# Performance work log

Hardware: AMD Instinct MI355X
Metric: run time of the kernel (lower is better)

Reference implementation:

```python
import jax, jax.numpy as jnp
import numpy as np

EPS = 1e-5
NEG_SLOPE = 0.2  # torch LeakyReLU default in DGCNN-style SharedMLPs


def knn_idx(p, k):
    # p: [B, 3, N]; returns idx [B, N, k] of k nearest neighbors (incl. self)
    inner = jnp.einsum('bdn,bdm->bnm', p, p)           # [B,N,N]
    sq = jnp.sum(p * p, axis=1)                         # [B,N]
    neg_dist = 2.0 * inner - sq[:, :, None] - sq[:, None, :]
    return jax.lax.top_k(neg_dist, k)[1]                # [B,N,k]


def smlp1d(x, w, b, g, bt):
    # x: [B,C,N]; 1x1 conv + BatchNorm1d (batch stats) + LeakyReLU
    y = jnp.einsum('bcn,oc->bon', x, w) + b[None, :, None]
    m = y.mean(axis=(0, 2), keepdims=True)
    v = y.var(axis=(0, 2), keepdims=True)
    y = g[None, :, None] * (y - m) * jax.lax.rsqrt(v + EPS) + bt[None, :, None]
    return jax.nn.leaky_relu(y, NEG_SLOPE)


def edgeconv(x, idx, w, b, g, bt):
    # x: [B,C,N], idx: [B,N,k] -> [B,O,N]
    B = x.shape[0]
    xT = jnp.transpose(x, (0, 2, 1))                    # [B,N,C]
    nb = xT[jnp.arange(B)[:, None, None], idx]          # [B,N,k,C] gather
    ctr = jnp.broadcast_to(xT[:, :, None, :], nb.shape)
    feat = jnp.concatenate([nb - ctr, ctr], axis=-1)    # [B,N,k,2C]
    y = jnp.einsum('bnkc,oc->bnko', feat, w) + b        # 1x1 conv2d
    m = y.mean(axis=(0, 1, 2), keepdims=True)
    v = y.var(axis=(0, 1, 2), keepdims=True)
    y = g * (y - m) * jax.lax.rsqrt(v + EPS) + bt
    y = jax.nn.leaky_relu(y, NEG_SLOPE)
    y = jnp.max(y, axis=2)                              # max over k -> [B,N,O]
    return jnp.transpose(y, (0, 2, 1))                  # [B,O,N]


def setup_inputs() -> dict:
    key = jax.random.key(0)
    ks = jax.random.split(key, 16)
    B, N, K = 2, 8192, 20
    C_in = 1024 + 3 * 64  # emb_dims + n_edgeconvs_backbone*64 = 1216
    OUT = 50

    def lin(k, o, c):
        return jax.random.normal(k, (o, c), jnp.float32) * (1.0 / np.sqrt(c))

    return {
        'x': jax.random.normal(ks[0], (B, C_in, N), jnp.float32),
        'p': jax.random.normal(ks[1], (B, 3, N), jnp.float32),
        # smlp1: 1216 -> 256
        'w1': lin(ks[2], 256, C_in), 'b1': jnp.zeros((256,), jnp.float32),
        'g1': jnp.ones((256,), jnp.float32), 'bt1': jnp.zeros((256,), jnp.float32),
        # edgeconv: 512 -> 256
        'we': lin(ks[3], 256, 512), 'be': jnp.zeros((256,), jnp.float32),
        'ge': jnp.ones((256,), jnp.float32), 'bte': jnp.zeros((256,), jnp.float32),
        # smlp2 part 1: 256 -> 256
        'w2': lin(ks[4], 256, 256), 'b2': jnp.zeros((256,), jnp.float32),
        'g2': jnp.ones((256,), jnp.float32), 'bt2': jnp.zeros((256,), jnp.float32),
        # smlp2 part 2: 256 -> 128
        'w3': lin(ks[5], 128, 256), 'b3': jnp.zeros((128,), jnp.float32),
        'g3': jnp.ones((128,), jnp.float32), 'bt3': jnp.zeros((128,), jnp.float32),
        # final conv1d: 128 -> 50
        'wf': lin(ks[6], OUT, 128), 'bf': jnp.zeros((OUT,), jnp.float32),
    }


def reference(x, p, w1, b1, g1, bt1, we, be, ge, bte,
              w2, b2, g2, bt2, w3, b3, g3, bt3, wf, bf):
    K = 20
    h = smlp1d(x, w1, b1, g1, bt1)              # [B,256,N]
    idx = knn_idx(p, K)                          # [B,N,K]
    h = edgeconv(h, idx, we, be, ge, bte)        # [B,256,N]
    h = smlp1d(h, w2, b2, g2, bt2)               # Dropout2d: identity (eval)
    h = smlp1d(h, w3, b3, g3, bt3)               # [B,128,N]
    return jnp.einsum('bcn,oc->bon', h, wf) + bf[None, :, None]  # [B,50,N]
```

## Files before the change

kernel.cpp:

```cpp
#include <hip/hip_runtime.h>

typedef unsigned short u16;
typedef unsigned int   u32;
typedef unsigned long long u64;
typedef __attribute__((ext_vector_type(4))) float f4;
typedef __attribute__((ext_vector_type(8))) short s8;
typedef __attribute__((ext_vector_type(4))) int   i4v;
typedef __attribute__((ext_vector_type(4))) unsigned short u16x4;

#define DEV __device__ __forceinline__

DEV u16 f2b(float f) {
  u32 u = __float_as_uint(f);
  return (u16)((u + 0x7FFFu + ((u >> 16) & 1u)) >> 16);
}
DEV float b2f(u16 h) { return __uint_as_float(((u32)h) << 16); }

#define OFF_STATS 0L
#define OFF_W1B   65536L
#define OFF_WEAB  688128L
#define OFF_W2B   950272L
#define OFF_W3B   1081344L
#define OFF_IDX   1146880L
#define OFF_XT    4194304L
#define OFF_Y1    44040192L
#define OFF_Y2    4194304L
#define OFF_EMAX  23068672L
#define OFF_EMIN  41943040L
#define OFF_Y3    4194304L
#define OFF_Y4    23068672L
#define WS_NEED   71303168L

__global__ __launch_bounds__(256) void k_convw(
    const float* __restrict__ w1, const float* __restrict__ we,
    const float* __restrict__ w2, const float* __restrict__ w3,
    u16* __restrict__ w1b, u16* __restrict__ weABb,
    u16* __restrict__ w2b, u16* __restrict__ w3b)
{
  int i = blockIdx.x * 256 + threadIdx.x;
  if (i < 311296) { w1b[i] = f2b(w1[i]); return; }
  i -= 311296;
  if (i < 131072) {
    int o = i >> 8, c = i & 255;
    float v = (o < 256) ? we[o * 512 + c]
                        : we[(o - 256) * 512 + 256 + c] - we[(o - 256) * 512 + c];
    weABb[i] = f2b(v); return;
  }
  i -= 131072;
  if (i < 65536) { w2b[i] = f2b(w2[i]); return; }
  i -= 65536;
  if (i < 32768) { w3b[i] = f2b(w3[i]); }
}

__global__ __launch_bounds__(256) void k_xt(const float* __restrict__ x, u16* __restrict__ xt)
{
  __shared__ float t[64][65];
  const int b = blockIdx.z, ct = blockIdx.y, nt = blockIdx.x;
  const int tx = threadIdx.x & 63, ty = threadIdx.x >> 6;
  const float* xb = x + (long)b * 1216 * 8192;
#pragma unroll
  for (int i = 0; i < 16; ++i) {
    int c = ct * 64 + ty + i * 4;
    t[ty + i * 4][tx] = xb[(long)c * 8192 + nt * 64 + tx];
  }
  __syncthreads();
  u16* xtb = xt + (long)b * 8192 * 1216;
#pragma unroll
  for (int i = 0; i < 16; ++i) {
    int n = nt * 64 + ty + i * 4;
    xtb[(long)n * 1216 + ct * 64 + tx] = f2b(t[tx][ty + i * 4]);
  }
}

__global__ __launch_bounds__(512, 1) void k_knn(const float* __restrict__ p, int* __restrict__ idxOut)
{
  __shared__ f4 pq[8192];
  __shared__ u16 cand[8][8][120];
  __shared__ double ckeyv[8][120];
  const int tid = threadIdx.x, lane = tid & 63, w = tid >> 6;
  const int blk = blockIdx.x;
  const int b = blk >> 7;
  const int qbase = ((blk & 127) << 6) + (w << 3);
  const float* px = p + (long)b * 24576;
  const float* py = px + 8192;
  const float* pz = px + 16384;
  for (int t4 = tid; t4 < 2048; t4 += 512) {
    f4 x4 = *(const f4*)(px + t4 * 4);
    f4 y4 = *(const f4*)(py + t4 * 4);
    f4 z4 = *(const f4*)(pz + t4 * 4);
#pragma unroll
    for (int j = 0; j < 4; ++j) {
      float X = x4[j], Yv = y4[j], Z = z4[j];
      float s = fmaf(X, X, fmaf(Yv, Yv, Z * Z));
      f4 v; v[0] = X; v[1] = Yv; v[2] = Z; v[3] = s;
      pq[t4 * 4 + j] = v;
    }
  }
  __syncthreads();
  float qx2[8], qy2[8], qz2[8];
#pragma unroll
  for (int j = 0; j < 8; ++j) {
    f4 Q = pq[qbase + j];
    qx2[j] = Q[0] + Q[0]; qy2[j] = Q[1] + Q[1]; qz2[j] = Q[2] + Q[2];
  }
  float mx[8];
#pragma unroll
  for (int j = 0; j < 8; ++j) mx[j] = -3.0e38f;
#pragma unroll 4
  for (int t = 0; t < 128; ++t) {
    f4 c = pq[(t << 6) + lane];
#pragma unroll
    for (int j = 0; j < 8; ++j) {
      float v = fmaf(qx2[j], c[0], fmaf(qy2[j], c[1], fmaf(qz2[j], c[2], -c[3])));
      mx[j] = fmaxf(mx[j], v);
    }
  }
  float sv[8];
#pragma unroll
  for (int j = 0; j < 8; ++j) sv[j] = mx[j];
#pragma unroll
  for (int k = 2; k <= 64; k <<= 1) {
#pragma unroll
    for (int s = k >> 1; s > 0; s >>= 1) {
      const bool takeMin = (((lane & k) == 0) == ((lane & s) == 0));
#pragma unroll
      for (int j = 0; j < 8; ++j) {
        float o = __shfl_xor(sv[j], s);
        sv[j] = takeMin ? fminf(sv[j], o) : fmaxf(sv[j], o);
      }
    }
  }
  float T[8];
#pragma unroll
  for (int j = 0; j < 8; ++j) T[j] = __shfl(sv[j], 44) - 1e-3f;
  int cnt[8];
#pragma unroll
  for (int j = 0; j < 8; ++j) cnt[j] = 0;
#pragma unroll 4
  for (int t = 0; t < 128; ++t) {
    f4 c = pq[(t << 6) + lane];
#pragma unroll
    for (int j = 0; j < 8; ++j) {
      float v = fmaf(qx2[j], c[0], fmaf(qy2[j], c[1], fmaf(qz2[j], c[2], -c[3])));
      bool pr = (v >= T[j]);
      u64 ball = __ballot(pr);
      if (ball) {
        int ofs = (int)__popcll(ball & ((1ull << lane) - 1ull));
        int pos = cnt[j] + ofs;
        if (pr && pos < 120) cand[w][j][pos] = (u16)((t << 6) + lane);
        cnt[j] += (int)__popcll(ball);
      }
    }
  }
  asm volatile("s_waitcnt lgkmcnt(0)" ::: "memory");
  for (int j = 0; j < 8; ++j) {
    const int cn = cnt[j] > 120 ? 120 : cnt[j];
    f4 Q = pq[qbase + j];
    const double Qx = (double)Q[0], Qy = (double)Q[1], Qz = (double)Q[2];
    const double Qs = Qx * Qx + Qy * Qy + Qz * Qz;
    double myV[2]; int myI[2];
#pragma unroll
    for (int jj = 0; jj < 2; ++jj) {
      const int e = lane + (jj << 6);
      myV[jj] = -1.0e300; myI[jj] = 0x7FFFFFFF;
      if (e < cn) {
        const int ci = cand[w][j][e];
        f4 c = pq[ci];
        double cx = (double)c[0], cy = (double)c[1], cz = (double)c[2];
        double v = 2.0 * (Qx * cx + Qy * cy + Qz * cz) - Qs - (cx * cx + cy * cy + cz * cz);
        myV[jj] = v; myI[jj] = ci;
        ckeyv[w][e] = v;
      }
    }
    asm volatile("s_waitcnt lgkmcnt(0)" ::: "memory");
    int rk0 = 0, rk1 = 0;
#pragma unroll 4
    for (int e2 = 0; e2 < cn; ++e2) {
      double ov = ckeyv[w][e2];
      int oi = (int)cand[w][j][e2];
      rk0 += ((ov > myV[0]) || (ov == myV[0] && oi < myI[0])) ? 1 : 0;
      rk1 += ((ov > myV[1]) || (ov == myV[1] && oi < myI[1])) ? 1 : 0;
    }
    int* orow = idxOut + (((long)b << 13) + qbase + j) * 20;
    if (lane < cn && rk0 < 20) orow[rk0] = myI[0];
    if (lane + 64 < cn && rk1 < 20) orow[rk1] = myI[1];
  }
}

DEV float lky(float z) { return z > 0.f ? z : 0.2f * z; }

DEV i4v applyPack8(f4 a, f4 b4, const float* sc, const float* sh, int kb) {
  u16 r[8];
#pragma unroll
  for (int e = 0; e < 4; ++e) r[e] = f2b(lky(fmaf(sc[kb + e], a[e], sh[kb + e])));
#pragma unroll
  for (int e = 0; e < 4; ++e) r[4 + e] = f2b(lky(fmaf(sc[kb + 4 + e], b4[e], sh[kb + 4 + e])));
  i4v o;
#pragma unroll
  for (int e = 0; e < 4; ++e) o[e] = (int)((u32)r[2 * e] | ((u32)r[2 * e + 1] << 16));
  return o;
}

DEV i4v selPack8(f4 a, f4 b4, f4 a2, f4 b2, const float* sc, const float* sh, int kb) {
  u16 r[8];
#pragma unroll
  for (int e = 0; e < 4; ++e) {
    float s = sc[kb + e];
    float y = (s >= 0.f) ? a[e] : a2[e];
    r[e] = f2b(lky(fmaf(s, y, sh[kb + e])));
  }
#pragma unroll
  for (int e = 0; e < 4; ++e) {
    float s = sc[kb + 4 + e];
    float y = (s >= 0.f) ? b4[e] : b2[e];
    r[4 + e] = f2b(lky(fmaf(s, y, sh[kb + 4 + e])));
  }
  i4v o;
#pragma unroll
  for (int e = 0; e < 4; ++e) o[e] = (int)((u32)r[2 * e] | ((u32)r[2 * e + 1] << 16));
  return o;
}

template<int BMODE, int STATS, int BF16OUT>
__global__ __launch_bounds__(256, 2) void k_gemm(
    const u16* __restrict__ A, const void* __restrict__ B0v, const void* __restrict__ B1v,
    const float* __restrict__ sums, const float* __restrict__ ssq,
    const float* __restrict__ g, const float* __restrict__ bt, float invCount,
    float* __restrict__ gsums, float* __restrict__ gssq,
    void* __restrict__ Yv, int M, int K, long strideB, long strideY)
{
  __shared__ u16 sA[2][4096];
  __shared__ u16 sB[2][4096];
  __shared__ float scB[256], shB[256];
  __shared__ float s_sum[128], s_ssq[128];
  const int b = blockIdx.z;
  const int m0 = blockIdx.y * 128;
  const int n0 = blockIdx.x * 128;
  const int tid = threadIdx.x, lane = tid & 63, w = tid >> 6;
  const int wr = w >> 1, wc = w & 1;
  const int r15 = lane & 15, g8 = (lane >> 4) * 8;

  if (BMODE != 0) {
    float m = sums[tid] * invCount;
    float v = ssq[tid] * invCount - m * m;
    float s = g[tid] / sqrtf(v + 1e-5f);
    scB[tid] = s;
    shB[tid] = bt[tid] - m * s;
  }
  if (STATS) { if (tid < 128) { s_sum[tid] = 0.f; s_ssq[tid] = 0.f; } }
  if (BMODE != 0) __syncthreads();

  f4 acc[4][4];
#pragma unroll
  for (int i = 0; i < 4; ++i)
#pragma unroll
    for (int j = 0; j < 4; ++j) { f4 z = {0.f, 0.f, 0.f, 0.f}; acc[i][j] = z; }

  const int row0 = tid >> 2;
  const int kp0 = (tid & 3) << 3;
  const u16* gA0 = A + (long)(m0 + row0) * K + kp0;
  const u16* gA1 = A + (long)(m0 + row0 + 64) * K + kp0;
  const int ch0 = tid, ch1 = tid + 256;

  const u16* gB0 = (const u16*)B0v + (long)b * strideB + (long)(n0 + row0) * K + kp0;
  const u16* gB1 = gB0 + (long)64 * K;
  const float* fB0 = (const float*)B0v + (long)b * strideB + (long)(n0 + row0) * K + kp0;
  const float* fB1 = fB0 + (long)64 * K;
  const float* eB0 = (const float*)B1v + (long)b * strideB + (long)(n0 + row0) * K + kp0;
  const float* eB1 = eB0 + (long)64 * K;

  ((i4v*)sA[0])[ch0] = *(const i4v*)gA0;
  ((i4v*)sA[0])[ch1] = *(const i4v*)gA1;
  if (BMODE == 0) {
    ((i4v*)sB[0])[ch0] = *(const i4v*)gB0;
    ((i4v*)sB[0])[ch1] = *(const i4v*)gB1;
  } else if (BMODE == 1) {
    ((i4v*)sB[0])[ch0] = applyPack8(*(const f4*)fB0, *(const f4*)(fB0 + 4), scB, shB, kp0);
    ((i4v*)sB[0])[ch1] = applyPack8(*(const f4*)fB1, *(const f4*)(fB1 + 4), scB, shB, kp0);
  } else {
    ((i4v*)sB[0])[ch0] = selPack8(*(const f4*)fB0, *(const f4*)(fB0 + 4),
                                  *(const f4*)eB0, *(const f4*)(eB0 + 4), scB, shB, kp0);
    ((i4v*)sB[0])[ch1] = selPack8(*(const f4*)fB1, *(const f4*)(fB1 + 4),
                                  *(const f4*)eB1, *(const f4*)(eB1 + 4), scB, shB, kp0);
  }
  __syncthreads();

  const int KT = K >> 5;
  int cur = 0;
  for (int kk = 0; kk < KT; ++kk) {
    const bool more = (kk + 1 < KT);
    i4v ra0, ra1, rb0, rb1;
    f4 p0a, p0b, p1a, p1b, q0a, q0b, q1a, q1b;
    if (more) {
      long ko = (long)(kk + 1) * 32;
      ra0 = *(const i4v*)(gA0 + ko); ra1 = *(const i4v*)(gA1 + ko);
      if (BMODE == 0) {
        rb0 = *(const i4v*)(gB0 + ko); rb1 = *(const i4v*)(gB1 + ko);
      } else {
        p0a = *(const f4*)(fB0 + ko); p0b = *(const f4*)(fB0 + ko + 4);
        p1a = *(const f4*)(fB1 + ko); p1b = *(const f4*)(fB1 + ko + 4);
        if (BMODE == 2) {
          q0a = *(const f4*)(eB0 + ko); q0b = *(const f4*)(eB0 + ko + 4);
          q1a = *(const f4*)(eB1 + ko); q1b = *(const f4*)(eB1 + ko + 4);
        }
      }
    }
    const u16* la = sA[cur];
    const u16* lb = sB[cur];
    s8 af[4], bfr[4];
#pragma unroll
    for (int mi = 0; mi < 4; ++mi)
      af[mi] = *(const s8*)(la + (wr * 64 + mi * 16 + r15) * 32 + g8);
#pragma unroll
    for (int ni = 0; ni < 4; ++ni)
      bfr[ni] = *(const s8*)(lb + (wc * 64 + ni * 16 + r15) * 32 + g8);
#pragma unroll
    for (int mi = 0; mi < 4; ++mi)
#pragma unroll
      for (int ni = 0; ni < 4; ++ni)
        acc[mi][ni] = __builtin_amdgcn_mfma_f32_16x16x32_bf16(af[mi], bfr[ni], acc[mi][ni], 0, 0, 0);
    if (more) {
      ((i4v*)sA[cur ^ 1])[ch0] = ra0; ((i4v*)sA[cur ^ 1])[ch1] = ra1;
      if (BMODE == 0) {
        ((i4v*)sB[cur ^ 1])[ch0] = rb0; ((i4v*)sB[cur ^ 1])[ch1] = rb1;
      } else {
        const int kb = (kk + 1) * 32 + kp0;
        if (BMODE == 1) {
          ((i4v*)sB[cur ^ 1])[ch0] = applyPack8(p0a, p0b, scB, shB, kb);
          ((i4v*)sB[cur ^ 1])[ch1] = applyPack8(p1a, p1b, scB, shB, kb);
        } else {
          ((i4v*)sB[cur ^ 1])[ch0] = selPack8(p0a, p0b, q0a, q0b, scB, shB, kb);
          ((i4v*)sB[cur ^ 1])[ch1] = selPack8(p1a, p1b, q1a, q1b, scB, shB, kb);
        }
      }
    }
    __syncthreads();
    cur ^= 1;
  }
  const int og = m0 + wr * 64 + (lane >> 4) * 4;
  const int ng = n0 + wc * 64 + r15;
  if (BF16OUT) {
    u16* Yp = (u16*)Yv + (long)b * strideY;
#pragma unroll
    for (int mi = 0; mi < 4; ++mi)
#pragma unroll
      for (int ni = 0; ni < 4; ++ni) {
        f4 a = acc[mi][ni];
        u16x4 r;
#pragma unroll
        for (int q = 0; q < 4; ++q) r[q] = f2b(a[q]);
        *(u16x4*)(Yp + (long)(ng + ni * 16) * M + og + mi * 16) = r;
      }
  } else {
    float* Yp = (float*)Yv + (long)b * strideY;
#pragma unroll
    for (int mi = 0; mi < 4; ++mi)
#pragma unroll
      for (int ni = 0; ni < 4; ++ni)
        *(f4*)(Yp + (long)(ng + ni * 16) * M + og + mi * 16) = acc[mi][ni];
  }
  if (STATS) {
#pragma unroll
    for (int mi = 0; mi < 4; ++mi)
#pragma unroll
      for (int j = 0; j < 4; ++j) {
        float s = 0.f, q = 0.f;
#pragma unroll
        for (int ni = 0; ni < 4; ++ni) {
          float v = acc[mi][ni][j];
          s += v; q = fmaf(v, v, q);
        }
#pragma unroll
        for (int off = 1; off < 16; off <<= 1) {
          s += __shfl_xor(s, off);
          q += __shfl_xor(q, off);
        }
        if ((lane & 15) == 0) {
          int lc = wr * 64 + (lane >> 4) * 4 + mi * 16 + j;
          atomicAdd(&s_sum[lc], s);
          atomicAdd(&s_ssq[lc], q);
        }
      }
    __syncthreads();
    if (tid < 128) {
      atomicAdd(&gsums[m0 + tid], s_sum[tid]);
      atomicAdd(&gssq[m0 + tid], s_ssq[tid]);
    }
  }
}

__global__ __launch_bounds__(256, 2) void k_edge_gather(
    const u16* __restrict__ Y2, const int* __restrict__ idx,
    float* __restrict__ Emax, float* __restrict__ Emin,
    float* __restrict__ sums, float* __restrict__ ssq)
{
  __shared__ float s_sum[256], s_ssq[256];
  const int tid = threadIdx.x, lane = tid & 63, w = tid >> 6;
  s_sum[tid] = 0.f; s_ssq[tid] = 0.f;
  __syncthreads();
  const int ptBase = blockIdx.x * 64;
  f4 lsum = {0.f, 0.f, 0.f, 0.f}, lssq = {0.f, 0.f, 0.f, 0.f};
  for (int i = 0; i < 16; ++i) {
    const int pt = ptBase + w * 16 + i;
    const int b = pt >> 13;
    u16x4 cr = *(const u16x4*)(Y2 + (long)pt * 512 + 256 + (lane << 2));
    f4 ctr; ctr[0] = b2f(cr[0]); ctr[1] = b2f(cr[1]); ctr[2] = b2f(cr[2]); ctr[3] = b2f(cr[3]);
    const int* irow = idx + (long)pt * 20;
    f4 vmax = {-3.0e38f, -3.0e38f, -3.0e38f, -3.0e38f};
    f4 vmin = {3.0e38f, 3.0e38f, 3.0e38f, 3.0e38f};
#pragma unroll 4
    for (int k = 0; k < 20; ++k) {
      int m = irow[k];
      u16x4 nr = *(const u16x4*)(Y2 + (((long)b << 13) + m) * 512 + (lane << 2));
#pragma unroll
      for (int j = 0; j < 4; ++j) {
        float y = b2f(nr[j]) + ctr[j];
        vmax[j] = fmaxf(vmax[j], y);
        vmin[j] = fminf(vmin[j], y);
        lsum[j] += y;
        lssq[j] = fmaf(y, y, lssq[j]);
      }
    }
    *(f4*)(Emax + (long)pt * 256 + (lane << 2)) = vmax;
    *(f4*)(Emin + (long)pt * 256 + (lane << 2)) = vmin;
  }
#pragma unroll
  for (int j = 0; j < 4; ++j) {
    atomicAdd(&s_sum[(lane << 2) + j], lsum[j]);
    atomicAdd(&s_ssq[(lane << 2) + j], lssq[j]);
  }
  __syncthreads();
  atomicAdd(&sums[tid], s_sum[tid]);
  atomicAdd(&ssq[tid], s_ssq[tid]);
}

__global__ __launch_bounds__(64) void k_final(
    const float* __restrict__ Y4, const float* __restrict__ sums, const float* __restrict__ ssq,
    const float* __restrict__ g, const float* __restrict__ bt,
    const float* __restrict__ wf, const float* __restrict__ bf,
    float* __restrict__ out)
{
  __shared__ float swf[128][56];
  __shared__ float sc[128], sh[128], sb[52];
  const int lane = threadIdx.x;
  if (lane < 50) {
    const float* wrow = wf + lane * 128;
#pragma unroll 8
    for (int ch = 0; ch < 128; ++ch) swf[ch][lane] = wrow[ch];
    sb[lane] = bf[lane];
  } else if (lane < 52) {
#pragma unroll 8
    for (int ch = 0; ch < 128; ++ch) swf[ch][lane] = 0.f;
    sb[lane] = 0.f;
  }
#pragma unroll
  for (int t = 0; t < 2; ++t) {
    int ch = lane + t * 64;
    float m = sums[ch] * (1.0f / 16384.0f);
    float v = ssq[ch] * (1.0f / 16384.0f) - m * m;
    float s = g[ch] / sqrtf(v + 1e-5f);
    sc[ch] = s;
    sh[ch] = bt[ch] - m * s;
  }
  __syncthreads();
  const int b = blockIdx.y;
  const int n = blockIdx.x * 64 + lane;
  const float* hp = Y4 + ((long)b * 8192 + n) * 128;
  f4 av[13];
#pragma unroll
  for (int i = 0; i < 13; ++i) { f4 z = {0.f, 0.f, 0.f, 0.f}; av[i] = z; }
#pragma unroll 4
  for (int c4 = 0; c4 < 32; ++c4) {
    f4 hv = *(const f4*)(hp + c4 * 4);
#pragma unroll
    for (int e = 0; e < 4; ++e) {
      const int ch = c4 * 4 + e;
      float z = lky(fmaf(sc[ch], hv[e], sh[ch]));
#pragma unroll
      for (int o4 = 0; o4 < 13; ++o4) {
        f4 wv = *(const f4*)&swf[ch][o4 * 4];
#pragma unroll
        for (int q = 0; q < 4; ++q) av[o4][q] = fmaf(z, wv[q], av[o4][q]);
      }
    }
  }
  float* ob = out + (((long)b * 50) << 13) + n;
#pragma unroll
  for (int o4 = 0; o4 < 13; ++o4)
#pragma unroll
    for (int q = 0; q < 4; ++q) {
      int o = o4 * 4 + q;
      if (o < 50) ob[(long)o << 13] = av[o4][q] + sb[o];
    }
}

extern "C" void kernel_launch(void* const* d_in, const int* in_sizes, int n_in,
                              void* d_out, int out_size, void* d_ws, size_t ws_size,
                              hipStream_t stream)
{
  if ((long)ws_size < WS_NEED) return;
  const float* x   = (const float*)d_in[0];
  const float* p   = (const float*)d_in[1];
  const float* w1  = (const float*)d_in[2];
  const float* g1w = (const float*)d_in[4];
  const float* bt1 = (const float*)d_in[5];
  const float* we  = (const float*)d_in[6];
  const float* gew = (const float*)d_in[8];
  const float* bte = (const float*)d_in[9];
  const float* w2  = (const float*)d_in[10];
  const float* g2w = (const float*)d_in[12];
  const float* bt2 = (const float*)d_in[13];
  const float* w3  = (const float*)d_in[14];
  const float* g3w = (const float*)d_in[16];
  const float* bt3 = (const float*)d_in[17];
  const float* wf  = (const float*)d_in[18];
  const float* bfi = (const float*)d_in[19];

  char* ws = (char*)d_ws;
  u16* w1b   = (u16*)(ws + OFF_W1B);
  u16* weABb = (u16*)(ws + OFF_WEAB);
  u16* w2b   = (u16*)(ws + OFF_W2B);
  u16* w3b   = (u16*)(ws + OFF_W3B);
  int* idxb  = (int*)(ws + OFF_IDX);
  u16*   XT   = (u16*)(ws + OFF_XT);
  float* Y1   = (float*)(ws + OFF_Y1);
  u16*   Y2b  = (u16*)(ws + OFF_Y2);
  float* EMAX = (float*)(ws + OFF_EMAX);
  float* EMIN = (float*)(ws + OFF_EMIN);
  float* Y3   = (float*)(ws + OFF_Y3);
  float* Y4   = (float*)(ws + OFF_Y4);
  float* st0 = (float*)(ws + OFF_STATS);
  float* st1 = (float*)(ws + OFF_STATS + 4096);
  float* st2 = (float*)(ws + OFF_STATS + 8192);
  float* st3 = (float*)(ws + OFF_STATS + 12288);

  hipMemsetAsync(ws + OFF_STATS, 0, 16384, stream);
  k_convw<<<2112, 256, 0, stream>>>(w1, we, w2, w3, w1b, weABb, w2b, w3b);
  k_knn<<<256, 512, 0, stream>>>(p, idxb);
  k_xt<<<dim3(128, 19, 2), 256, 0, stream>>>(x, XT);

  k_gemm<0, 1, 0><<<dim3(64, 2, 2), 256, 0, stream>>>(
      w1b, XT, nullptr, nullptr, nullptr, nullptr, nullptr, 0.f,
      st0, st0 + 256, Y1, 256, 1216, (long)8192 * 1216, (long)8192 * 256);

  k_gemm<1, 0, 1><<<dim3(64, 4, 2), 256, 0, stream>>>(
      weABb, Y1, nullptr, st0, st0 + 256, g1w, bt1, 1.0f / 16384.0f,
      nullptr, nullptr, Y2b, 512, 256, (long)8192 * 256, (long)8192 * 512);

  k_edge_gather<<<256, 256, 0, stream>>>(Y2b, idxb, EMAX, EMIN, st1, st1 + 256);

  k_gemm<2, 1, 0><<<dim3(64, 2, 2), 256, 0, stream>>>(
      w2b, EMAX, EMIN, st1, st1 + 256, gew, bte, 1.0f / 327680.0f,
      st2, st2 + 256, Y3, 256, 256, (long)8192 * 256, (long)8192 * 256);

  k_gemm<1, 1, 0><<<dim3(64, 1, 2), 256, 0, stream>>>(
      w3b, Y3, nullptr, st2, st2 + 256, g2w, bt2, 1.0f / 16384.0f,
      st3, st3 + 256, Y4, 128, 256, (long)8192 * 256, (long)8192 * 128);

  k_final<<<dim3(128, 2), 64, 0, stream>>>(Y4, st3, st3 + 256, g3w, bt3, wf, bfi, (float*)d_out);
}
```

Measured before the change: 263.4 us.

## Restructure kNN to read global point buffer with smaller blocks and atomic compaction

Adds a prep kernel that packs points into an xyz+norm f4 buffer in global memory. The kNN kernel drops its 128KB LDS copy of all points and reads candidates straight from global/L2, with 4 queries per wave and 256-thread blocks, so it launches 1024 blocks instead of 256 and gets higher occupancy. Candidate compaction moves from ballot/popcount to LDS atomics with a 128-entry buffer. The cost is repeated global reads of the point set, plus ordering of candidates that is no longer deterministic, which the rank-based selection tolerates.

```diff
diff --git a/kernel.cpp b/kernel.cpp
--- a/kernel.cpp
+++ b/kernel.cpp
@@ -22,6 +22,7 @@
 #define OFF_W2B   950272L
 #define OFF_W3B   1081344L
 #define OFF_IDX   1146880L
+#define OFF_PQ    2457600L
 #define OFF_XT    4194304L
 #define OFF_Y1    44040192L
 #define OFF_Y2    4194304L
@@ -52,6 +53,16 @@
   if (i < 32768) { w3b[i] = f2b(w3[i]); }
 }
 
+__global__ __launch_bounds__(256) void k_prep(const float* __restrict__ p, f4* __restrict__ pqg)
+{
+  int i = blockIdx.x * 256 + threadIdx.x;
+  int b = i >> 13, n = i & 8191;
+  const float* pb = p + (long)b * 24576;
+  float X = pb[n], Y = pb[8192 + n], Z = pb[16384 + n];
+  f4 v; v[0] = X; v[1] = Y; v[2] = Z; v[3] = fmaf(X, X, fmaf(Y, Y, Z * Z));
+  pqg[i] = v;
+}
+
 __global__ __launch_bounds__(256) void k_xt(const float* __restrict__ x, u16* __restrict__ xt)
 {
   __shared__ float t[64][65];
@@ -72,90 +83,70 @@
   }
 }
 
-__global__ __launch_bounds__(512, 1) void k_knn(const float* __restrict__ p, int* __restrict__ idxOut)
-{
-  __shared__ f4 pq[8192];
-  __shared__ u16 cand[8][8][120];
-  __shared__ double ckeyv[8][120];
+__global__ __launch_bounds__(256) void k_knn(const f4* __restrict__ pqg, int* __restrict__ idxOut)
+{
+  __shared__ u16 cand[4][4][128];
+  __shared__ double ckeyv[4][128];
+  __shared__ int scnt[4][4];
   const int tid = threadIdx.x, lane = tid & 63, w = tid >> 6;
   const int blk = blockIdx.x;
-  const int b = blk >> 7;
-  const int qbase = ((blk & 127) << 6) + (w << 3);
-  const float* px = p + (long)b * 24576;
-  const float* py = px + 8192;
-  const float* pz = px + 16384;
-  for (int t4 = tid; t4 < 2048; t4 += 512) {
-    f4 x4 = *(const f4*)(px + t4 * 4);
-    f4 y4 = *(const f4*)(py + t4 * 4);
-    f4 z4 = *(const f4*)(pz + t4 * 4);
-#pragma unroll
-    for (int j = 0; j < 4; ++j) {
-      float X = x4[j], Yv = y4[j], Z = z4[j];
-      float s = fmaf(X, X, fmaf(Yv, Yv, Z * Z));
-      f4 v; v[0] = X; v[1] = Yv; v[2] = Z; v[3] = s;
-      pq[t4 * 4 + j] = v;
-    }
-  }
-  __syncthreads();
-  float qx2[8], qy2[8], qz2[8];
-#pragma unroll
-  for (int j = 0; j < 8; ++j) {
-    f4 Q = pq[qbase + j];
+  const int b = blk >> 9;
+  const int qbase = ((blk & 511) << 4) + (w << 2);
+  const f4* __restrict__ P = pqg + ((long)b << 13);
+  if (lane < 4) scnt[w][lane] = 0;
+  float qx2[4], qy2[4], qz2[4];
+#pragma unroll
+  for (int j = 0; j < 4; ++j) {
+    f4 Q = P[qbase + j];
     qx2[j] = Q[0] + Q[0]; qy2[j] = Q[1] + Q[1]; qz2[j] = Q[2] + Q[2];
   }
-  float mx[8];
-#pragma unroll
-  for (int j = 0; j < 8; ++j) mx[j] = -3.0e38f;
+  float mx[4];
+#pragma unroll
+  for (int j = 0; j < 4; ++j) mx[j] = -3.0e38f;
 #pragma unroll 4
   for (int t = 0; t < 128; ++t) {
-    f4 c = pq[(t << 6) + lane];
-#pragma unroll
-    for (int j = 0; j < 8; ++j) {
+    f4 c = P[(t << 6) + lane];
+#pragma unroll
+    for (int j = 0; j < 4; ++j) {
       float v = fmaf(qx2[j], c[0], fmaf(qy2[j], c[1], fmaf(qz2[j], c[2], -c[3])));
       mx[j] = fmaxf(mx[j], v);
     }
   }
-  float sv[8];
-#pragma unroll
-  for (int j = 0; j < 8; ++j) sv[j] = mx[j];
+  float sv[4];
+#pragma unroll
+  for (int j = 0; j < 4; ++j) sv[j] = mx[j];
 #pragma unroll
   for (int k = 2; k <= 64; k <<= 1) {
 #pragma unroll
     for (int s = k >> 1; s > 0; s >>= 1) {
       const bool takeMin = (((lane & k) == 0) == ((lane & s) == 0));
 #pragma unroll
-      for (int j = 0; j < 8; ++j) {
+      for (int j = 0; j < 4; ++j) {
         float o = __shfl_xor(sv[j], s);
         sv[j] = takeMin ? fminf(sv[j], o) : fmaxf(sv[j], o);
       }
     }
   }
-  float T[8];
-#pragma unroll
-  for (int j = 0; j < 8; ++j) T[j] = __shfl(sv[j], 44) - 1e-3f;
-  int cnt[8];
-#pragma unroll
-  for (int j = 0; j < 8; ++j) cnt[j] = 0;
-#pragma unroll 4
+  float T[4];
+#pragma unroll
+  for (int j = 0; j < 4; ++j) T[j] = __shfl(sv[j], 44) - 1e-3f;
+  asm volatile("s_waitcnt lgkmcnt(0)" ::: "memory");
+#pragma unroll 2
   for (int t = 0; t < 128; ++t) {
-    f4 c = pq[(t << 6) + lane];
-#pragma unroll
-    for (int j = 0; j < 8; ++j) {
+    f4 c = P[(t << 6) + lane];
+#pragma unroll
+    for (int j = 0; j < 4; ++j) {
       float v = fmaf(qx2[j], c[0], fmaf(qy2[j], c[1], fmaf(qz2[j], c[2], -c[3])));
-      bool pr = (v >= T[j]);
-      u64 ball = __ballot(pr);
-      if (ball) {
-        int ofs = (int)__popcll(ball & ((1ull << lane) - 1ull));
-        int pos = cnt[j] + ofs;
-        if (pr && pos < 120) cand[w][j][pos] = (u16)((t << 6) + lane);
-        cnt[j] += (int)__popcll(ball);
+      if (v >= T[j]) {
+        int pos = atomicAdd(&scnt[w][j], 1);
+        if (pos < 128) cand[w][j][pos] = (u16)((t << 6) + lane);
       }
     }
   }
   asm volatile("s_waitcnt lgkmcnt(0)" ::: "memory");
-  for (int j = 0; j < 8; ++j) {
-    const int cn = cnt[j] > 120 ? 120 : cnt[j];
-    f4 Q = pq[qbase + j];
+  for (int j = 0; j < 4; ++j) {
+    int cn = scnt[w][j]; if (cn > 128) cn = 128;
+    f4 Q = P[qbase + j];
     const double Qx = (double)Q[0], Qy = (double)Q[1], Qz = (double)Q[2];
     const double Qs = Qx * Qx + Qy * Qy + Qz * Qz;
     double myV[2]; int myI[2];
@@ -165,7 +156,7 @@
       myV[jj] = -1.0e300; myI[jj] = 0x7FFFFFFF;
       if (e < cn) {
         const int ci = cand[w][j][e];
-        f4 c = pq[ci];
+        f4 c = P[ci];
         double cx = (double)c[0], cy = (double)c[1], cz = (double)c[2];
         double v = 2.0 * (Qx * cx + Qy * cy + Qz * cz) - Qs - (cx * cx + cy * cy + cz * cz);
         myV[jj] = v; myI[jj] = ci;
@@ -184,6 +175,7 @@
     int* orow = idxOut + (((long)b << 13) + qbase + j) * 20;
     if (lane < cn && rk0 < 20) orow[rk0] = myI[0];
     if (lane + 64 < cn && rk1 < 20) orow[rk1] = myI[1];
+    asm volatile("s_waitcnt lgkmcnt(0)" ::: "memory");
   }
 }
 
@@ -522,6 +514,7 @@
   u16* w2b   = (u16*)(ws + OFF_W2B);
   u16* w3b   = (u16*)(ws + OFF_W3B);
   int* idxb  = (int*)(ws + OFF_IDX);
+  f4*  pqg   = (f4*)(ws + OFF_PQ);
   u16*   XT   = (u16*)(ws + OFF_XT);
   float* Y1   = (float*)(ws + OFF_Y1);
   u16*   Y2b  = (u16*)(ws + OFF_Y2);
@@ -536,7 +529,8 @@
 
   hipMemsetAsync(ws + OFF_STATS, 0, 16384, stream);
   k_convw<<<2112, 256, 0, stream>>>(w1, we, w2, w3, w1b, weABb, w2b, w3b);
-  k_knn<<<256, 512, 0, stream>>>(p, idxb);
+  k_prep<<<64, 256, 0, stream>>>(p, pqg);
+  k_knn<<<1024, 256, 0, stream>>>(pqg, idxb);
   k_xt<<<dim3(128, 19, 2), 256, 0, stream>>>(x, XT);
 
   k_gemm<0, 1, 0><<<dim3(64, 2, 2), 256, 0, stream>>>(
```

After: 259.2 us. No clear change (-1.6%).
